# Performance work log

Hardware: AMD Instinct MI355X
Metric: run time of the kernel (lower is better)

The kernel has to match this reference:

```python
import jax, jax.numpy as jnp
import numpy as np

N_HEADS = 8
D_EMBED = 512
D_CROSS = 768
D_HEAD = D_EMBED // N_HEADS


def setup_inputs() -> dict:
    key = jax.random.key(0)
    ks = jax.random.split(key, 12)
    B, SQ, SKV = 8, 4096, 77
    s_e = 1.0 / np.sqrt(D_EMBED)
    s_c = 1.0 / np.sqrt(D_CROSS)
    return {
        "latent": jax.random.normal(ks[0], (B, SQ, D_EMBED), jnp.float32),
        "context": jax.random.normal(ks[1], (B, SKV, D_CROSS), jnp.float32),
        "wq": jax.random.normal(ks[2], (D_EMBED, D_EMBED), jnp.float32) * s_e,
        "bq": jax.random.normal(ks[3], (D_EMBED,), jnp.float32) * 0.01,
        "wk": jax.random.normal(ks[4], (D_CROSS, D_EMBED), jnp.float32) * s_c,
        "bk": jax.random.normal(ks[5], (D_EMBED,), jnp.float32) * 0.01,
        "wv": jax.random.normal(ks[6], (D_CROSS, D_EMBED), jnp.float32) * s_c,
        "bv": jax.random.normal(ks[7], (D_EMBED,), jnp.float32) * 0.01,
        "wo": jax.random.normal(ks[8], (D_EMBED, D_EMBED), jnp.float32) * s_e,
        "bo": jax.random.normal(ks[9], (D_EMBED,), jnp.float32) * 0.01,
    }


def reference(latent, context, wq, bq, wk, bk, wv, bv, wo, bo):
    B, SQ, _ = latent.shape
    SKV = context.shape[1]
    # projections; weights stored as (in, out)
    q = latent @ wq + bq                     # [B, SQ, D_EMBED]
    k = context @ wk + bk                    # [B, SKV, D_EMBED]
    v = context @ wv + bv                    # [B, SKV, D_EMBED]
    # split heads -> [B, H, S, Dh]
    q = q.reshape(B, SQ, N_HEADS, D_HEAD).transpose(0, 2, 1, 3)
    k = k.reshape(B, SKV, N_HEADS, D_HEAD).transpose(0, 2, 1, 3)
    v = v.reshape(B, SKV, N_HEADS, D_HEAD).transpose(0, 2, 1, 3)
    scale = 1.0 / np.sqrt(D_HEAD).astype(np.float32)
    w = jnp.einsum("bhqd,bhkd->bhqk", q, k) * scale  # [B, H, SQ, SKV]
    w = jax.nn.softmax(w, axis=-1)
    out = jnp.einsum("bhqk,bhkd->bhqd", w, v)        # [B, H, SQ, Dh]
    out = out.transpose(0, 2, 1, 3).reshape(B, SQ, D_EMBED)
    return out @ wo + bo
```

## Files before the change

kernel.cpp:

```cpp
#include <hip/hip_runtime.h>


typedef __attribute__((ext_vector_type(8))) __bf16 bf16x8;
typedef __attribute__((ext_vector_type(4))) float f32x4;

#define DEVI static __device__ __forceinline__

typedef __attribute__((address_space(3))) void lds_void_t;
typedef const __attribute__((address_space(1))) void gbl_void_t;
#define GLDS16(gsrc, ldst) \
  __builtin_amdgcn_global_load_lds((gbl_void_t*)(gsrc), (lds_void_t*)(ldst), 16, 0, 0)

DEVI unsigned short f2bf(float f) {
  unsigned int u = __float_as_uint(f);
  u += 0x7FFFu + ((u >> 16) & 1u);
  return (unsigned short)(u >> 16);
}

DEVI unsigned int pack2bf(float a, float b) {
  return (unsigned int)f2bf(a) | ((unsigned int)f2bf(b) << 16);
}

__global__ __launch_bounds__(256) void prep_kernel(
    const float* __restrict__ wq, const float* __restrict__ wk,
    const float* __restrict__ wv, const float* __restrict__ wo,
    unsigned short* __restrict__ wqT, unsigned short* __restrict__ wkT,
    unsigned short* __restrict__ wvT, unsigned short* __restrict__ woT,
    const float* __restrict__ latent, unsigned int* __restrict__ latBF4) {
  int bid = blockIdx.x;
  int tid = threadIdx.x;
  if (bid >= 1280) {
    size_t i = (size_t)(bid - 1280) * 256 + tid;
    const float4* in4 = (const float4*)latent;
    float4 a = in4[2 * i];
    float4 b = in4[2 * i + 1];
    uint4 o;
    o.x = pack2bf(a.x, a.y);
    o.y = pack2bf(a.z, a.w);
    o.z = pack2bf(b.x, b.y);
    o.w = pack2bf(b.z, b.w);
    *(uint4*)(latBF4 + 4 * i) = o;
    return;
  }
  __shared__ float tile[32][33];
  const float* in;
  unsigned short* out;
  int K, r;
  if (bid < 256)       { in = wq; out = wqT; K = 512; r = bid; }
  else if (bid < 640)  { in = wk; out = wkT; K = 768; r = bid - 256; }
  else if (bid < 1024) { in = wv; out = wvT; K = 768; r = bid - 640; }
  else                 { in = wo; out = woT; K = 512; r = bid - 1024; }
  int n0 = (r & 15) * 32, k0 = (r >> 4) * 32;
  int tx = tid & 31, ty = tid >> 5;
#pragma unroll
  for (int j = 0; j < 4; ++j)
    tile[ty * 4 + j][tx] = in[(size_t)(k0 + ty * 4 + j) * 512 + n0 + tx];
  __syncthreads();
#pragma unroll
  for (int j = 0; j < 4; ++j)
    out[(size_t)(n0 + ty * 4 + j) * K + k0 + tx] = f2bf(tile[tx][ty * 4 + j]);
}

__global__ __launch_bounds__(256) void kv_proj_kernel(const float* __restrict__ ctx,
                                                      const unsigned short* __restrict__ wkT,
                                                      const unsigned short* __restrict__ wvT,
                                                      const float* __restrict__ bk,
                                                      const float* __restrict__ bv,
                                                      unsigned short* __restrict__ Kp,
                                                      unsigned short* __restrict__ Vt) {
  __shared__ __align__(16) unsigned short As[64][40];
  __shared__ __align__(16) unsigned short Bs[64][40];
  int bid = blockIdx.x;
  int sel = bid / 80;
  int rem = bid % 80;
  int mt = rem / 8, nt = rem % 8;
  const unsigned short* wT = sel ? wvT : wkT;
  const float* bias = sel ? bv : bk;
  int tid = threadIdx.x;
  int l = tid & 63, w = tid >> 6;
  int lr = l & 15, lg = l >> 4;

  f32x4 acc[4] = {};
  for (int k0 = 0; k0 < 768; k0 += 32) {
#pragma unroll
    for (int it = 0; it < 2; ++it) {
      int idx4 = it * 256 + tid;
      int r = idx4 >> 3, q4 = idx4 & 7;
      int m = mt * 64 + r;
      float4 v = {0.f, 0.f, 0.f, 0.f};
      if (m < 616) v = *(const float4*)(ctx + (size_t)m * 768 + k0 + q4 * 4);
      ushort4 o;
      o.x = f2bf(v.x); o.y = f2bf(v.y); o.z = f2bf(v.z); o.w = f2bf(v.w);
      *(ushort4*)&As[r][q4 * 4] = o;
    }
    {
      int c = tid >> 2, q8 = tid & 3;
      *(uint4*)&Bs[c][q8 * 8] =
          *(const uint4*)(wT + (size_t)(nt * 64 + c) * 768 + k0 + q8 * 8);
    }
    __syncthreads();
    bf16x8 a = *(const bf16x8*)&As[w * 16 + lr][lg * 8];
#pragma unroll
    for (int n = 0; n < 4; ++n) {
      bf16x8 bb = *(const bf16x8*)&Bs[n * 16 + lr][lg * 8];
      acc[n] = __builtin_amdgcn_mfma_f32_16x16x32_bf16(a, bb, acc[n], 0, 0, 0);
    }
    __syncthreads();
  }
#pragma unroll
  for (int n = 0; n < 4; ++n) {
#pragma unroll
    for (int reg = 0; reg < 4; ++reg) {
      int m = mt * 64 + w * 16 + lg * 4 + reg;
      if (m < 616) {
        int bI = m / 77, s = m % 77;
        int col = nt * 64 + n * 16 + lr;
        int h = col >> 6, d = col & 63;
        float v = acc[n][reg] + bias[col];
        if (sel == 0)
          Kp[(((size_t)(bI * 8 + h)) * 80 + s) * 64 + d] = f2bf(v);
        else
          Vt[(((size_t)(bI * 8 + h)) * 64 + d) * 96 + s] = f2bf(v);
      }
    }
  }
}

#define KSTEP(t, boff)                                                        \
  {                                                                           \
    if ((t) < 15)                                                             \
      asm volatile("s_waitcnt vmcnt(4)" ::: "memory");                        \
    else                                                                      \
      asm volatile("s_waitcnt vmcnt(0)" ::: "memory");                        \
    __builtin_amdgcn_s_barrier();                                             \
    __builtin_amdgcn_sched_barrier(0);                                        \
    const unsigned short* bufA = smem + (boff);                               \
    const unsigned short* bufB = bufA + 4096;                                 \
    bf16x8 af[4], bv8[4];                                                     \
    _Pragma("unroll") for (int m = 0; m < 4; ++m)                             \
        af[m] = *(const bf16x8*)&bufA[(wr + m * 16 + lr) * 32 + lg * 8];      \
    _Pragma("unroll") for (int n = 0; n < 4; ++n)                             \
        bv8[n] = *(const bf16x8*)&bufB[(wc + n * 16 + lr) * 32 + lg * 8];     \
    asm volatile("s_waitcnt lgkmcnt(0)" ::: "memory");                        \
    __builtin_amdgcn_sched_barrier(0);                                        \
    __builtin_amdgcn_s_barrier();                                             \
    if ((t) <= 13) {                                                          \
      int nk = ((t) + 2) * 32;                                                \
      GLDS16(gA + nk, smem + (boff) + w * 1024);                              \
      GLDS16(gA + nk + 16 * 512, smem + (boff) + w * 1024 + 512);             \
      GLDS16(gB + nk, smem + (boff) + 4096 + w * 1024);                       \
      GLDS16(gB + nk + 16 * 512, smem + (boff) + 4096 + w * 1024 + 512);      \
    }                                                                         \
    _Pragma("unroll") for (int m = 0; m < 4; ++m)                             \
        _Pragma("unroll") for (int n = 0; n < 4; ++n)                         \
            acc[m][n] = __builtin_amdgcn_mfma_f32_16x16x32_bf16(              \
                af[m], bv8[n], acc[m][n], 0, 0, 0);                           \
  }

__global__ __launch_bounds__(256, 4) void qproj_attn_kernel(
    const unsigned short* __restrict__ A, const unsigned short* __restrict__ BT,
    const float* __restrict__ bias, const unsigned short* __restrict__ Kp,
    const unsigned short* __restrict__ Vt, unsigned short* __restrict__ Oq) {
  __shared__ __align__(16) unsigned short smem[18432];

  int bid = ((blockIdx.x & 7) << 7) | (blockIdx.x >> 3);
  size_t mbase = (size_t)(bid >> 2) * 128;
  int nbase = (bid & 3) * 128;
  int tid = threadIdx.x;
  int l = tid & 63, w = tid >> 6;
  int lr = l & 15, lg = l >> 4;
  int wr = (w >> 1) * 64, wc = (w & 1) * 64;

  const unsigned short* gA = A + (mbase + w * 32 + (l >> 2)) * 512 + (l & 3) * 8;
  const unsigned short* gB = BT + (size_t)(nbase + w * 32 + (l >> 2)) * 512 + (l & 3) * 8;

  GLDS16(gA, smem + w * 1024);
  GLDS16(gA + 16 * 512, smem + w * 1024 + 512);
  GLDS16(gB, smem + 4096 + w * 1024);
  GLDS16(gB + 16 * 512, smem + 4096 + w * 1024 + 512);
  GLDS16(gA + 32, smem + 8192 + w * 1024);
  GLDS16(gA + 32 + 16 * 512, smem + 8192 + w * 1024 + 512);
  GLDS16(gB + 32, smem + 12288 + w * 1024);
  GLDS16(gB + 32 + 16 * 512, smem + 12288 + w * 1024 + 512);

  f32x4 acc[4][4] = {};
#pragma unroll 1
  for (int t = 0; t < 16; t += 2) {
    KSTEP(t, 0);
    KSTEP(t + 1, 8192);
  }

  unsigned short* Qme = smem + w * (64 * 72);
  float bb[4];
#pragma unroll
  for (int n = 0; n < 4; ++n) bb[n] = bias[nbase + wc + n * 16 + lr];
#pragma unroll
  for (int m = 0; m < 4; ++m)
#pragma unroll
    for (int n = 0; n < 4; ++n)
#pragma unroll
      for (int reg = 0; reg < 4; ++reg)
        Qme[(m * 16 + lg * 4 + reg) * 72 + n * 16 + lr] = f2bf(acc[m][n][reg] + bb[n]);

  bf16x8 qf[4][2];
#pragma unroll
  for (int rg = 0; rg < 4; ++rg) {
    qf[rg][0] = *(const bf16x8*)&Qme[(rg * 16 + lr) * 72 + lg * 8];
    qf[rg][1] = *(const bf16x8*)&Qme[(rg * 16 + lr) * 72 + 32 + lg * 8];
  }

  unsigned short* Pme = Qme;
  for (int z = l; z < 256; z += 64) Pme[(z >> 4) * 104 + 80 + (z & 15)] = 0;

  int b = (int)(mbase >> 12);
  int h = (bid & 3) * 2 + (w & 1);
  const unsigned short* Kph = Kp + (size_t)(b * 8 + h) * (80 * 64);
  const unsigned short* Vth = Vt + (size_t)(b * 8 + h) * (64 * 96);

  const float C = 0.125f * 1.44269504088896f;

  auto QK = [&](int rg, f32x4* s) {
#pragma unroll
    for (int t = 0; t < 5; ++t) {
      const unsigned short* kr = Kph + (t * 16 + lr) * 64 + lg * 8;
      bf16x8 k0 = *(const bf16x8*)kr;
      bf16x8 k1 = *(const bf16x8*)(kr + 32);
      s[t] = __builtin_amdgcn_mfma_f32_16x16x32_bf16(qf[rg][0], k0, s[t], 0, 0, 0);
      s[t] = __builtin_amdgcn_mfma_f32_16x16x32_bf16(qf[rg][1], k1, s[t], 0, 0, 0);
    }
    if (lr >= 13) {
      s[4][0] = -1e30f; s[4][1] = -1e30f; s[4][2] = -1e30f; s[4][3] = -1e30f;
    }
  };

  f32x4 sc[5] = {};
  QK(0, sc);
#pragma unroll
  for (int rg = 0; rg < 4; ++rg) {
    float mx[4];
#pragma unroll
    for (int r = 0; r < 4; ++r)
      mx[r] = fmaxf(fmaxf(fmaxf(sc[0][r], sc[1][r]), fmaxf(sc[2][r], sc[3][r])), sc[4][r]);
#pragma unroll
    for (int d = 1; d < 16; d <<= 1)
#pragma unroll
      for (int r = 0; r < 4; ++r) mx[r] = fmaxf(mx[r], __shfl_xor(mx[r], d, 64));
    float p[5][4];
#pragma unroll
    for (int t = 0; t < 5; ++t)
#pragma unroll
      for (int r = 0; r < 4; ++r) p[t][r] = exp2f((sc[t][r] - mx[r]) * C);
#pragma unroll
    for (int t = 0; t < 5; ++t)
#pragma unroll
      for (int r = 0; r < 4; ++r)
        Pme[(lg * 4 + r) * 104 + t * 16 + lr] = f2bf(p[t][r]);

    float sm[4];
#pragma unroll
    for (int r = 0; r < 4; ++r)
      sm[r] = p[0][r] + p[1][r] + p[2][r] + p[3][r] + p[4][r];
#pragma unroll
    for (int d = 1; d < 16; d <<= 1)
#pragma unroll
      for (int r = 0; r < 4; ++r) sm[r] += __shfl_xor(sm[r], d, 64);
    float rs[4];
#pragma unroll
    for (int r = 0; r < 4; ++r) rs[r] = 1.0f / sm[r];

    f32x4 sn[5] = {};
    if (rg < 3) QK(rg + 1, sn);

    bf16x8 ap[3];
#pragma unroll
    for (int c = 0; c < 3; ++c) ap[c] = *(const bf16x8*)&Pme[lr * 104 + c * 32 + lg * 8];
#pragma unroll
    for (int ct = 0; ct < 4; ++ct) {
      f32x4 o = {};
#pragma unroll
      for (int c = 0; c < 3; ++c) {
        bf16x8 vv = *(const bf16x8*)(Vth + (size_t)(ct * 16 + lr) * 96 + c * 32 + lg * 8);
        o = __builtin_amdgcn_mfma_f32_16x16x32_bf16(ap[c], vv, o, 0, 0, 0);
      }
#pragma unroll
      for (int reg = 0; reg < 4; ++reg)
        Oq[(mbase + wr + rg * 16 + lg * 4 + reg) * 512 + nbase + wc + ct * 16 + lr] =
            f2bf(o[reg] * rs[reg]);
    }
#pragma unroll
    for (int t = 0; t < 5; ++t) sc[t] = sn[t];
  }
}

__global__ __launch_bounds__(256) void gemm512_glds_kernel(
    const unsigned short* __restrict__ A, const unsigned short* __restrict__ BT,
    const float* __restrict__ bias, float* __restrict__ Out) {
  __shared__ __align__(16) unsigned short smem[16384];
  int bid = ((blockIdx.x & 7) << 7) | (blockIdx.x >> 3);
  size_t mbase = (size_t)(bid >> 2) * 128;
  int nbase = (bid & 3) * 128;
  int tid = threadIdx.x;
  int l = tid & 63, w = tid >> 6;
  int lr = l & 15, lg = l >> 4;
  int wr = (w >> 1) * 64, wc = (w & 1) * 64;

  const unsigned short* gA = A + (mbase + w * 32 + (l >> 2)) * 512 + (l & 3) * 8;
  const unsigned short* gB = BT + (size_t)(nbase + w * 32 + (l >> 2)) * 512 + (l & 3) * 8;

  GLDS16(gA, smem + w * 1024);
  GLDS16(gA + 16 * 512, smem + w * 1024 + 512);
  GLDS16(gB, smem + 4096 + w * 1024);
  GLDS16(gB + 16 * 512, smem + 4096 + w * 1024 + 512);
  GLDS16(gA + 32, smem + 8192 + w * 1024);
  GLDS16(gA + 32 + 16 * 512, smem + 8192 + w * 1024 + 512);
  GLDS16(gB + 32, smem + 12288 + w * 1024);
  GLDS16(gB + 32 + 16 * 512, smem + 12288 + w * 1024 + 512);

  f32x4 acc[4][4] = {};
#pragma unroll 1
  for (int t = 0; t < 16; t += 2) {
    KSTEP(t, 0);
    KSTEP(t + 1, 8192);
  }

#pragma unroll
  for (int m = 0; m < 4; ++m) {
#pragma unroll
    for (int n = 0; n < 4; ++n) {
#pragma unroll
      for (int reg = 0; reg < 4; ++reg) {
        size_t row = mbase + wr + m * 16 + lg * 4 + reg;
        int col = nbase + wc + n * 16 + lr;
        Out[row * 512 + col] = acc[m][n][reg] + bias[col];
      }
    }
  }
}

static const size_t OFF_Q   = 0;
static const size_t OFF_KP  = 33554432;
static const size_t OFF_VT  = OFF_KP + 655360;
static const size_t OFF_WQT = OFF_VT + 786432;
static const size_t OFF_WKT = OFF_WQT + 524288;
static const size_t OFF_WVT = OFF_WKT + 786432;
static const size_t OFF_WOT = OFF_WVT + 786432;
static const size_t WS_NEEDED = OFF_WOT + 524288;

extern "C" void kernel_launch(void* const* d_in, const int* in_sizes, int n_in,
                              void* d_out, int out_size, void* d_ws, size_t ws_size,
                              hipStream_t stream) {
  (void)in_sizes; (void)n_in; (void)out_size;
  if (ws_size < WS_NEEDED) return;

  const float* latent  = (const float*)d_in[0];
  const float* context = (const float*)d_in[1];
  const float* wq = (const float*)d_in[2];
  const float* bq = (const float*)d_in[3];
  const float* wk = (const float*)d_in[4];
  const float* bk = (const float*)d_in[5];
  const float* wv = (const float*)d_in[6];
  const float* bv = (const float*)d_in[7];
  const float* wo = (const float*)d_in[8];
  const float* bo = (const float*)d_in[9];
  float* out = (float*)d_out;

  char* ws = (char*)d_ws;
  unsigned short* wsQ = (unsigned short*)(ws + OFF_Q);
  unsigned short* Kp  = (unsigned short*)(ws + OFF_KP);
  unsigned short* Vt  = (unsigned short*)(ws + OFF_VT);
  unsigned short* wqT = (unsigned short*)(ws + OFF_WQT);
  unsigned short* wkT = (unsigned short*)(ws + OFF_WKT);
  unsigned short* wvT = (unsigned short*)(ws + OFF_WVT);
  unsigned short* woT = (unsigned short*)(ws + OFF_WOT);

  unsigned short* latBF = (unsigned short*)d_out;

  prep_kernel<<<1280 + 8192, 256, 0, stream>>>(wq, wk, wv, wo, wqT, wkT, wvT,
                                               woT, latent,
                                               (unsigned int*)latBF);
  hipMemsetAsync(ws + OFF_KP, 0, 655360 + 786432, stream);
  kv_proj_kernel<<<160, 256, 0, stream>>>(context, wkT, wvT, bk, bv, Kp, Vt);
  qproj_attn_kernel<<<1024, 256, 0, stream>>>(latBF, wqT, bq, Kp, Vt, wsQ);
  gemm512_glds_kernel<<<1024, 256, 0, stream>>>(wsQ, woT, bo, out);
}
```

Measured before the change: 125.1 us.

## Fuse latent fp32-to-bf16 conversion into Q-projection GEMM load path

Removes the separate pass that converted the whole latent tensor to bf16 (a read of 64MB fp32 and a write of 32MB bf16). The Q-projection attention kernel now streams fp32 latent tiles straight into LDS and converts them to bf16 in registers with the hardware packed-convert instruction just before the MFMAs. The cost is double the LDS footprint for the A tile, larger shared memory per block, and occupancy lowered from 4 to 3 blocks per CU. It also adds more LDS read traffic per k-step.

```diff
diff --git a/kernel.cpp b/kernel.cpp
--- a/kernel.cpp
+++ b/kernel.cpp
@@ -17,32 +17,29 @@
   return (unsigned short)(u >> 16);
 }
 
-DEVI unsigned int pack2bf(float a, float b) {
-  return (unsigned int)f2bf(a) | ((unsigned int)f2bf(b) << 16);
-}
-
-__global__ __launch_bounds__(256) void prep_kernel(
+DEVI unsigned int cvt_pk_bf16(float lo, float hi) {
+  unsigned int r;
+  asm("v_cvt_pk_bf16_f32 %0, %1, %2" : "=v"(r) : "v"(lo), "v"(hi));
+  return r;
+}
+
+DEVI bf16x8 cvt8(float4 a, float4 b) {
+  uint4 u;
+  u.x = cvt_pk_bf16(a.x, a.y);
+  u.y = cvt_pk_bf16(a.z, a.w);
+  u.z = cvt_pk_bf16(b.x, b.y);
+  u.w = cvt_pk_bf16(b.z, b.w);
+  return *(bf16x8*)&u;
+}
+
+__global__ __launch_bounds__(256) void wtrans_all_kernel(
     const float* __restrict__ wq, const float* __restrict__ wk,
     const float* __restrict__ wv, const float* __restrict__ wo,
     unsigned short* __restrict__ wqT, unsigned short* __restrict__ wkT,
-    unsigned short* __restrict__ wvT, unsigned short* __restrict__ woT,
-    const float* __restrict__ latent, unsigned int* __restrict__ latBF4) {
+    unsigned short* __restrict__ wvT, unsigned short* __restrict__ woT) {
+  __shared__ float tile[32][33];
   int bid = blockIdx.x;
   int tid = threadIdx.x;
-  if (bid >= 1280) {
-    size_t i = (size_t)(bid - 1280) * 256 + tid;
-    const float4* in4 = (const float4*)latent;
-    float4 a = in4[2 * i];
-    float4 b = in4[2 * i + 1];
-    uint4 o;
-    o.x = pack2bf(a.x, a.y);
-    o.y = pack2bf(a.z, a.w);
-    o.z = pack2bf(b.x, b.y);
-    o.w = pack2bf(b.z, b.w);
-    *(uint4*)(latBF4 + 4 * i) = o;
-    return;
-  }
-  __shared__ float tile[32][33];
   const float* in;
   unsigned short* out;
   int K, r;
@@ -123,6 +120,178 @@
           Vt[(((size_t)(bI * 8 + h)) * 64 + d) * 96 + s] = f2bf(v);
       }
     }
+  }
+}
+
+#define QSTEP(t, AO, BO)                                                      \
+  {                                                                           \
+    if ((t) < 15)                                                             \
+      asm volatile("s_waitcnt vmcnt(6)" ::: "memory");                        \
+    else                                                                      \
+      asm volatile("s_waitcnt vmcnt(0)" ::: "memory");                        \
+    __builtin_amdgcn_s_barrier();                                             \
+    __builtin_amdgcn_sched_barrier(0);                                        \
+    const float* Af = (const float*)(smem + (AO));                            \
+    const unsigned short* Bf = smem + (BO);                                   \
+    float4 ax[4], ay[4];                                                      \
+    bf16x8 bv8[4];                                                            \
+    _Pragma("unroll") for (int m = 0; m < 4; ++m) {                           \
+      ax[m] = *(const float4*)&Af[(wr + m * 16 + lr) * 32 + lg * 8];          \
+      ay[m] = *(const float4*)&Af[(wr + m * 16 + lr) * 32 + lg * 8 + 4];      \
+    }                                                                         \
+    _Pragma("unroll") for (int n = 0; n < 4; ++n)                             \
+        bv8[n] = *(const bf16x8*)&Bf[(wc + n * 16 + lr) * 32 + lg * 8];       \
+    asm volatile("s_waitcnt lgkmcnt(0)" ::: "memory");                        \
+    __builtin_amdgcn_sched_barrier(0);                                        \
+    __builtin_amdgcn_s_barrier();                                             \
+    if ((t) <= 13) {                                                          \
+      int nk = ((t) + 2) * 32;                                                \
+      _Pragma("unroll") for (int i = 0; i < 4; ++i)                           \
+          GLDS16(gA32 + nk + i * 4096, smem + (AO) + w * 2048 + i * 512);     \
+      GLDS16(gB + nk, smem + (BO) + w * 1024);                                \
+      GLDS16(gB + nk + 16 * 512, smem + (BO) + w * 1024 + 512);               \
+    }                                                                         \
+    bf16x8 af[4];                                                             \
+    _Pragma("unroll") for (int m = 0; m < 4; ++m) af[m] = cvt8(ax[m], ay[m]); \
+    _Pragma("unroll") for (int m = 0; m < 4; ++m)                             \
+        _Pragma("unroll") for (int n = 0; n < 4; ++n)                         \
+            acc[m][n] = __builtin_amdgcn_mfma_f32_16x16x32_bf16(              \
+                af[m], bv8[n], acc[m][n], 0, 0, 0);                           \
+  }
+
+__global__ __launch_bounds__(256, 3) void qproj_attn_kernel(
+    const float* __restrict__ A32, const unsigned short* __restrict__ BT,
+    const float* __restrict__ bias, const unsigned short* __restrict__ Kp,
+    const unsigned short* __restrict__ Vt, unsigned short* __restrict__ Oq) {
+  __shared__ __align__(16) unsigned short smem[24576];
+
+  int bid = ((blockIdx.x & 7) << 7) | (blockIdx.x >> 3);
+  size_t mbase = (size_t)(bid >> 2) * 128;
+  int nbase = (bid & 3) * 128;
+  int tid = threadIdx.x;
+  int l = tid & 63, w = tid >> 6;
+  int lr = l & 15, lg = l >> 4;
+  int wr = (w >> 1) * 64, wc = (w & 1) * 64;
+
+  const float* gA32 = A32 + (mbase + w * 32 + (l >> 3)) * 512 + (l & 7) * 4;
+  const unsigned short* gB = BT + (size_t)(nbase + w * 32 + (l >> 2)) * 512 + (l & 3) * 8;
+
+#pragma unroll
+  for (int i = 0; i < 4; ++i) GLDS16(gA32 + i * 4096, smem + w * 2048 + i * 512);
+  GLDS16(gB, smem + 8192 + w * 1024);
+  GLDS16(gB + 16 * 512, smem + 8192 + w * 1024 + 512);
+#pragma unroll
+  for (int i = 0; i < 4; ++i)
+    GLDS16(gA32 + 32 + i * 4096, smem + 12288 + w * 2048 + i * 512);
+  GLDS16(gB + 32, smem + 20480 + w * 1024);
+  GLDS16(gB + 32 + 16 * 512, smem + 20480 + w * 1024 + 512);
+
+  f32x4 acc[4][4] = {};
+#pragma unroll 1
+  for (int t = 0; t < 16; t += 2) {
+    QSTEP(t, 0, 8192);
+    QSTEP(t + 1, 12288, 20480);
+  }
+
+  unsigned short* Qme = smem + w * (64 * 72);
+  float bb[4];
+#pragma unroll
+  for (int n = 0; n < 4; ++n) bb[n] = bias[nbase + wc + n * 16 + lr];
+#pragma unroll
+  for (int m = 0; m < 4; ++m)
+#pragma unroll
+    for (int n = 0; n < 4; ++n)
+#pragma unroll
+      for (int reg = 0; reg < 4; ++reg)
+        Qme[(m * 16 + lg * 4 + reg) * 72 + n * 16 + lr] = f2bf(acc[m][n][reg] + bb[n]);
+
+  bf16x8 qf[4][2];
+#pragma unroll
+  for (int rg = 0; rg < 4; ++rg) {
+    qf[rg][0] = *(const bf16x8*)&Qme[(rg * 16 + lr) * 72 + lg * 8];
+    qf[rg][1] = *(const bf16x8*)&Qme[(rg * 16 + lr) * 72 + 32 + lg * 8];
+  }
+
+  unsigned short* Pme = Qme;
+  for (int z = l; z < 256; z += 64) Pme[(z >> 4) * 104 + 80 + (z & 15)] = 0;
+
+  int b = (int)(mbase >> 12);
+  int h = (bid & 3) * 2 + (w & 1);
+  const unsigned short* Kph = Kp + (size_t)(b * 8 + h) * (80 * 64);
+  const unsigned short* Vth = Vt + (size_t)(b * 8 + h) * (64 * 96);
+
+  const float C = 0.125f * 1.44269504088896f;
+
+  auto QK = [&](int rg, f32x4* s) {
+#pragma unroll
+    for (int t = 0; t < 5; ++t) {
+      const unsigned short* kr = Kph + (t * 16 + lr) * 64 + lg * 8;
+      bf16x8 k0 = *(const bf16x8*)kr;
+      bf16x8 k1 = *(const bf16x8*)(kr + 32);
+      s[t] = __builtin_amdgcn_mfma_f32_16x16x32_bf16(qf[rg][0], k0, s[t], 0, 0, 0);
+      s[t] = __builtin_amdgcn_mfma_f32_16x16x32_bf16(qf[rg][1], k1, s[t], 0, 0, 0);
+    }
+    if (lr >= 13) {
+      s[4][0] = -1e30f; s[4][1] = -1e30f; s[4][2] = -1e30f; s[4][3] = -1e30f;
+    }
+  };
+
+  f32x4 sc[5] = {};
+  QK(0, sc);
+#pragma unroll
+  for (int rg = 0; rg < 4; ++rg) {
+    float mx[4];
+#pragma unroll
+    for (int r = 0; r < 4; ++r)
+      mx[r] = fmaxf(fmaxf(fmaxf(sc[0][r], sc[1][r]), fmaxf(sc[2][r], sc[3][r])), sc[4][r]);
+#pragma unroll
+    for (int d = 1; d < 16; d <<= 1)
+#pragma unroll
+      for (int r = 0; r < 4; ++r) mx[r] = fmaxf(mx[r], __shfl_xor(mx[r], d, 64));
+    float p[5][4];
+#pragma unroll
+    for (int t = 0; t < 5; ++t)
+#pragma unroll
+      for (int r = 0; r < 4; ++r) p[t][r] = exp2f((sc[t][r] - mx[r]) * C);
+#pragma unroll
+    for (int t = 0; t < 5; ++t)
+#pragma unroll
+      for (int r = 0; r < 4; ++r)
+        Pme[(lg * 4 + r) * 104 + t * 16 + lr] = f2bf(p[t][r]);
+
+    float sm[4];
+#pragma unroll
+    for (int r = 0; r < 4; ++r)
+      sm[r] = p[0][r] + p[1][r] + p[2][r] + p[3][r] + p[4][r];
+#pragma unroll
+    for (int d = 1; d < 16; d <<= 1)
+#pragma unroll
+      for (int r = 0; r < 4; ++r) sm[r] += __shfl_xor(sm[r], d, 64);
+    float rs[4];
+#pragma unroll
+    for (int r = 0; r < 4; ++r) rs[r] = 1.0f / sm[r];
+
+    f32x4 sn[5] = {};
+    if (rg < 3) QK(rg + 1, sn);
+
+    bf16x8 ap[3];
+#pragma unroll
+    for (int c = 0; c < 3; ++c) ap[c] = *(const bf16x8*)&Pme[lr * 104 + c * 32 + lg * 8];
+#pragma unroll
+    for (int ct = 0; ct < 4; ++ct) {
+      f32x4 o = {};
+#pragma unroll
+      for (int c = 0; c < 3; ++c) {
+        bf16x8 vv = *(const bf16x8*)(Vth + (size_t)(ct * 16 + lr) * 96 + c * 32 + lg * 8);
+        o = __builtin_amdgcn_mfma_f32_16x16x32_bf16(ap[c], vv, o, 0, 0, 0);
+      }
+#pragma unroll
+      for (int reg = 0; reg < 4; ++reg)
+        Oq[(mbase + wr + rg * 16 + lg * 4 + reg) * 512 + nbase + wc + ct * 16 + lr] =
+            f2bf(o[reg] * rs[reg]);
+    }
+#pragma unroll
+    for (int t = 0; t < 5; ++t) sc[t] = sn[t];
   }
 }
 
@@ -157,141 +326,6 @@
                 af[m], bv8[n], acc[m][n], 0, 0, 0);                           \
   }
 
-__global__ __launch_bounds__(256, 4) void qproj_attn_kernel(
-    const unsigned short* __restrict__ A, const unsigned short* __restrict__ BT,
-    const float* __restrict__ bias, const unsigned short* __restrict__ Kp,
-    const unsigned short* __restrict__ Vt, unsigned short* __restrict__ Oq) {
-  __shared__ __align__(16) unsigned short smem[18432];
-
-  int bid = ((blockIdx.x & 7) << 7) | (blockIdx.x >> 3);
-  size_t mbase = (size_t)(bid >> 2) * 128;
-  int nbase = (bid & 3) * 128;
-  int tid = threadIdx.x;
-  int l = tid & 63, w = tid >> 6;
-  int lr = l & 15, lg = l >> 4;
-  int wr = (w >> 1) * 64, wc = (w & 1) * 64;
-
-  const unsigned short* gA = A + (mbase + w * 32 + (l >> 2)) * 512 + (l & 3) * 8;
-  const unsigned short* gB = BT + (size_t)(nbase + w * 32 + (l >> 2)) * 512 + (l & 3) * 8;
-
-  GLDS16(gA, smem + w * 1024);
-  GLDS16(gA + 16 * 512, smem + w * 1024 + 512);
-  GLDS16(gB, smem + 4096 + w * 1024);
-  GLDS16(gB + 16 * 512, smem + 4096 + w * 1024 + 512);
-  GLDS16(gA + 32, smem + 8192 + w * 1024);
-  GLDS16(gA + 32 + 16 * 512, smem + 8192 + w * 1024 + 512);
-  GLDS16(gB + 32, smem + 12288 + w * 1024);
-  GLDS16(gB + 32 + 16 * 512, smem + 12288 + w * 1024 + 512);
-
-  f32x4 acc[4][4] = {};
-#pragma unroll 1
-  for (int t = 0; t < 16; t += 2) {
-    KSTEP(t, 0);
-    KSTEP(t + 1, 8192);
-  }
-
-  unsigned short* Qme = smem + w * (64 * 72);
-  float bb[4];
-#pragma unroll
-  for (int n = 0; n < 4; ++n) bb[n] = bias[nbase + wc + n * 16 + lr];
-#pragma unroll
-  for (int m = 0; m < 4; ++m)
-#pragma unroll
-    for (int n = 0; n < 4; ++n)
-#pragma unroll
-      for (int reg = 0; reg < 4; ++reg)
-        Qme[(m * 16 + lg * 4 + reg) * 72 + n * 16 + lr] = f2bf(acc[m][n][reg] + bb[n]);
-
-  bf16x8 qf[4][2];
-#pragma unroll
-  for (int rg = 0; rg < 4; ++rg) {
-    qf[rg][0] = *(const bf16x8*)&Qme[(rg * 16 + lr) * 72 + lg * 8];
-    qf[rg][1] = *(const bf16x8*)&Qme[(rg * 16 + lr) * 72 + 32 + lg * 8];
-  }
-
-  unsigned short* Pme = Qme;
-  for (int z = l; z < 256; z += 64) Pme[(z >> 4) * 104 + 80 + (z & 15)] = 0;
-
-  int b = (int)(mbase >> 12);
-  int h = (bid & 3) * 2 + (w & 1);
-  const unsigned short* Kph = Kp + (size_t)(b * 8 + h) * (80 * 64);
-  const unsigned short* Vth = Vt + (size_t)(b * 8 + h) * (64 * 96);
-
-  const float C = 0.125f * 1.44269504088896f;
-
-  auto QK = [&](int rg, f32x4* s) {
-#pragma unroll
-    for (int t = 0; t < 5; ++t) {
-      const unsigned short* kr = Kph + (t * 16 + lr) * 64 + lg * 8;
-      bf16x8 k0 = *(const bf16x8*)kr;
-      bf16x8 k1 = *(const bf16x8*)(kr + 32);
-      s[t] = __builtin_amdgcn_mfma_f32_16x16x32_bf16(qf[rg][0], k0, s[t], 0, 0, 0);
-      s[t] = __builtin_amdgcn_mfma_f32_16x16x32_bf16(qf[rg][1], k1, s[t], 0, 0, 0);
-    }
-    if (lr >= 13) {
-      s[4][0] = -1e30f; s[4][1] = -1e30f; s[4][2] = -1e30f; s[4][3] = -1e30f;
-    }
-  };
-
-  f32x4 sc[5] = {};
-  QK(0, sc);
-#pragma unroll
-  for (int rg = 0; rg < 4; ++rg) {
-    float mx[4];
-#pragma unroll
-    for (int r = 0; r < 4; ++r)
-      mx[r] = fmaxf(fmaxf(fmaxf(sc[0][r], sc[1][r]), fmaxf(sc[2][r], sc[3][r])), sc[4][r]);
-#pragma unroll
-    for (int d = 1; d < 16; d <<= 1)
-#pragma unroll
-      for (int r = 0; r < 4; ++r) mx[r] = fmaxf(mx[r], __shfl_xor(mx[r], d, 64));
-    float p[5][4];
-#pragma unroll
-    for (int t = 0; t < 5; ++t)
-#pragma unroll
-      for (int r = 0; r < 4; ++r) p[t][r] = exp2f((sc[t][r] - mx[r]) * C);
-#pragma unroll
-    for (int t = 0; t < 5; ++t)
-#pragma unroll
-      for (int r = 0; r < 4; ++r)
-        Pme[(lg * 4 + r) * 104 + t * 16 + lr] = f2bf(p[t][r]);
-
-    float sm[4];
-#pragma unroll
-    for (int r = 0; r < 4; ++r)
-      sm[r] = p[0][r] + p[1][r] + p[2][r] + p[3][r] + p[4][r];
-#pragma unroll
-    for (int d = 1; d < 16; d <<= 1)
-#pragma unroll
-      for (int r = 0; r < 4; ++r) sm[r] += __shfl_xor(sm[r], d, 64);
-    float rs[4];
-#pragma unroll
-    for (int r = 0; r < 4; ++r) rs[r] = 1.0f / sm[r];
-
-    f32x4 sn[5] = {};
-    if (rg < 3) QK(rg + 1, sn);
-
-    bf16x8 ap[3];
-#pragma unroll
-    for (int c = 0; c < 3; ++c) ap[c] = *(const bf16x8*)&Pme[lr * 104 + c * 32 + lg * 8];
-#pragma unroll
-    for (int ct = 0; ct < 4; ++ct) {
-      f32x4 o = {};
-#pragma unroll
-      for (int c = 0; c < 3; ++c) {
-        bf16x8 vv = *(const bf16x8*)(Vth + (size_t)(ct * 16 + lr) * 96 + c * 32 + lg * 8);
-        o = __builtin_amdgcn_mfma_f32_16x16x32_bf16(ap[c], vv, o, 0, 0, 0);
-      }
-#pragma unroll
-      for (int reg = 0; reg < 4; ++reg)
-        Oq[(mbase + wr + rg * 16 + lg * 4 + reg) * 512 + nbase + wc + ct * 16 + lr] =
-            f2bf(o[reg] * rs[reg]);
-    }
-#pragma unroll
-    for (int t = 0; t < 5; ++t) sc[t] = sn[t];
-  }
-}
-
 __global__ __launch_bounds__(256) void gemm512_glds_kernel(
     const unsigned short* __restrict__ A, const unsigned short* __restrict__ BT,
     const float* __restrict__ bias, float* __restrict__ Out) {
@@ -373,13 +407,10 @@
   unsigned short* wvT = (unsigned short*)(ws + OFF_WVT);
   unsigned short* woT = (unsigned short*)(ws + OFF_WOT);
 
-  unsigned short* latBF = (unsigned short*)d_out;
-
-  prep_kernel<<<1280 + 8192, 256, 0, stream>>>(wq, wk, wv, wo, wqT, wkT, wvT,
-                                               woT, latent,
-                                               (unsigned int*)latBF);
+  wtrans_all_kernel<<<1280, 256, 0, stream>>>(wq, wk, wv, wo,
+                                              wqT, wkT, wvT, woT);
   hipMemsetAsync(ws + OFF_KP, 0, 655360 + 786432, stream);
   kv_proj_kernel<<<160, 256, 0, stream>>>(context, wkT, wvT, bk, bv, Kp, Vt);
-  qproj_attn_kernel<<<1024, 256, 0, stream>>>(latBF, wqT, bq, Kp, Vt, wsQ);
+  qproj_attn_kernel<<<1024, 256, 0, stream>>>(latent, wqT, bq, Kp, Vt, wsQ);
   gemm512_glds_kernel<<<1024, 256, 0, stream>>>(wsQ, woT, bo, out);
 }
```

Measured after the change: 119.4 us. 4.6% less time.

## XOR-swizzle LDS tiles in GEMMs and overlap latent conversion with KV projection

Applied to the files above, without the earlier changes.

Global-to-LDS loads and the MFMA fragment reads now use an XOR swizzle on the 16-byte column chunk. This is meant to cut LDS bank conflicts in the two 512-wide GEMM kernels. The latent fp32-to-bf16 conversion moves out of the weight-transpose kernel and into the KV projection launch. The 160 small KV-projection blocks therefore share a grid with the 8192 conversion blocks instead of running alone on a mostly idle GPU. The swizzle has to match exactly between writer lane mapping and reader indexing, or the results will be wrong.

```diff
diff --git a/kernel.cpp b/kernel.cpp
--- a/kernel.cpp
+++ b/kernel.cpp
@@ -21,16 +21,42 @@
   return (unsigned int)f2bf(a) | ((unsigned int)f2bf(b) << 16);
 }
 
-__global__ __launch_bounds__(256) void prep_kernel(
+__global__ __launch_bounds__(256) void wtrans_all_kernel(
     const float* __restrict__ wq, const float* __restrict__ wk,
     const float* __restrict__ wv, const float* __restrict__ wo,
     unsigned short* __restrict__ wqT, unsigned short* __restrict__ wkT,
-    unsigned short* __restrict__ wvT, unsigned short* __restrict__ woT,
-    const float* __restrict__ latent, unsigned int* __restrict__ latBF4) {
+    unsigned short* __restrict__ wvT, unsigned short* __restrict__ woT) {
+  __shared__ float tile[32][33];
   int bid = blockIdx.x;
   int tid = threadIdx.x;
-  if (bid >= 1280) {
-    size_t i = (size_t)(bid - 1280) * 256 + tid;
+  const float* in;
+  unsigned short* out;
+  int K, r;
+  if (bid < 256)       { in = wq; out = wqT; K = 512; r = bid; }
+  else if (bid < 640)  { in = wk; out = wkT; K = 768; r = bid - 256; }
+  else if (bid < 1024) { in = wv; out = wvT; K = 768; r = bid - 640; }
+  else                 { in = wo; out = woT; K = 512; r = bid - 1024; }
+  int n0 = (r & 15) * 32, k0 = (r >> 4) * 32;
+  int tx = tid & 31, ty = tid >> 5;
+#pragma unroll
+  for (int j = 0; j < 4; ++j)
+    tile[ty * 4 + j][tx] = in[(size_t)(k0 + ty * 4 + j) * 512 + n0 + tx];
+  __syncthreads();
+#pragma unroll
+  for (int j = 0; j < 4; ++j)
+    out[(size_t)(n0 + ty * 4 + j) * K + k0 + tx] = f2bf(tile[tx][ty * 4 + j]);
+}
+
+__global__ __launch_bounds__(256) void kv_cvt_kernel(
+    const float* __restrict__ ctx, const unsigned short* __restrict__ wkT,
+    const unsigned short* __restrict__ wvT, const float* __restrict__ bk,
+    const float* __restrict__ bv, unsigned short* __restrict__ Kp,
+    unsigned short* __restrict__ Vt, const float* __restrict__ latent,
+    unsigned int* __restrict__ latBF4) {
+  int bid0 = blockIdx.x;
+  int tid = threadIdx.x;
+  if (bid0 >= 160) {
+    size_t i = (size_t)(bid0 - 160) * 256 + tid;
     const float4* in4 = (const float4*)latent;
     float4 a = in4[2 * i];
     float4 b = in4[2 * i + 1];
@@ -42,41 +68,14 @@
     *(uint4*)(latBF4 + 4 * i) = o;
     return;
   }
-  __shared__ float tile[32][33];
-  const float* in;
-  unsigned short* out;
-  int K, r;
-  if (bid < 256)       { in = wq; out = wqT; K = 512; r = bid; }
-  else if (bid < 640)  { in = wk; out = wkT; K = 768; r = bid - 256; }
-  else if (bid < 1024) { in = wv; out = wvT; K = 768; r = bid - 640; }
-  else                 { in = wo; out = woT; K = 512; r = bid - 1024; }
-  int n0 = (r & 15) * 32, k0 = (r >> 4) * 32;
-  int tx = tid & 31, ty = tid >> 5;
-#pragma unroll
-  for (int j = 0; j < 4; ++j)
-    tile[ty * 4 + j][tx] = in[(size_t)(k0 + ty * 4 + j) * 512 + n0 + tx];
-  __syncthreads();
-#pragma unroll
-  for (int j = 0; j < 4; ++j)
-    out[(size_t)(n0 + ty * 4 + j) * K + k0 + tx] = f2bf(tile[tx][ty * 4 + j]);
-}
-
-__global__ __launch_bounds__(256) void kv_proj_kernel(const float* __restrict__ ctx,
-                                                      const unsigned short* __restrict__ wkT,
-                                                      const unsigned short* __restrict__ wvT,
-                                                      const float* __restrict__ bk,
-                                                      const float* __restrict__ bv,
-                                                      unsigned short* __restrict__ Kp,
-                                                      unsigned short* __restrict__ Vt) {
   __shared__ __align__(16) unsigned short As[64][40];
   __shared__ __align__(16) unsigned short Bs[64][40];
-  int bid = blockIdx.x;
+  int bid = bid0;
   int sel = bid / 80;
   int rem = bid % 80;
   int mt = rem / 8, nt = rem % 8;
   const unsigned short* wT = sel ? wvT : wkT;
   const float* bias = sel ? bv : bk;
-  int tid = threadIdx.x;
   int l = tid & 63, w = tid >> 6;
   int lr = l & 15, lg = l >> 4;
 
@@ -136,11 +135,14 @@
     __builtin_amdgcn_sched_barrier(0);                                        \
     const unsigned short* bufA = smem + (boff);                               \
     const unsigned short* bufB = bufA + 4096;                                 \
+    const int swB = (lr >> 1) & 3;                                            \
     bf16x8 af[4], bv8[4];                                                     \
     _Pragma("unroll") for (int m = 0; m < 4; ++m)                             \
-        af[m] = *(const bf16x8*)&bufA[(wr + m * 16 + lr) * 32 + lg * 8];      \
+        af[m] = *(const bf16x8*)&bufA[(wr + m * 16 + lr) * 32 +               \
+                                      (lg ^ swB) * 8];                        \
     _Pragma("unroll") for (int n = 0; n < 4; ++n)                             \
-        bv8[n] = *(const bf16x8*)&bufB[(wc + n * 16 + lr) * 32 + lg * 8];     \
+        bv8[n] = *(const bf16x8*)&bufB[(wc + n * 16 + lr) * 32 +              \
+                                       (lg ^ swB) * 8];                       \
     asm volatile("s_waitcnt lgkmcnt(0)" ::: "memory");                        \
     __builtin_amdgcn_sched_barrier(0);                                        \
     __builtin_amdgcn_s_barrier();                                             \
@@ -157,6 +159,16 @@
                 af[m], bv8[n], acc[m][n], 0, 0, 0);                           \
   }
 
+#define GEMM_PROLOGUE()                                                       \
+  GLDS16(gA, smem + w * 1024);                                                \
+  GLDS16(gA + 16 * 512, smem + w * 1024 + 512);                               \
+  GLDS16(gB, smem + 4096 + w * 1024);                                         \
+  GLDS16(gB + 16 * 512, smem + 4096 + w * 1024 + 512);                        \
+  GLDS16(gA + 32, smem + 8192 + w * 1024);                                    \
+  GLDS16(gA + 32 + 16 * 512, smem + 8192 + w * 1024 + 512);                   \
+  GLDS16(gB + 32, smem + 12288 + w * 1024);                                   \
+  GLDS16(gB + 32 + 16 * 512, smem + 12288 + w * 1024 + 512);
+
 __global__ __launch_bounds__(256, 4) void qproj_attn_kernel(
     const unsigned short* __restrict__ A, const unsigned short* __restrict__ BT,
     const float* __restrict__ bias, const unsigned short* __restrict__ Kp,
@@ -171,17 +183,12 @@
   int lr = l & 15, lg = l >> 4;
   int wr = (w >> 1) * 64, wc = (w & 1) * 64;
 
-  const unsigned short* gA = A + (mbase + w * 32 + (l >> 2)) * 512 + (l & 3) * 8;
-  const unsigned short* gB = BT + (size_t)(nbase + w * 32 + (l >> 2)) * 512 + (l & 3) * 8;
-
-  GLDS16(gA, smem + w * 1024);
-  GLDS16(gA + 16 * 512, smem + w * 1024 + 512);
-  GLDS16(gB, smem + 4096 + w * 1024);
-  GLDS16(gB + 16 * 512, smem + 4096 + w * 1024 + 512);
-  GLDS16(gA + 32, smem + 8192 + w * 1024);
-  GLDS16(gA + 32 + 16 * 512, smem + 8192 + w * 1024 + 512);
-  GLDS16(gB + 32, smem + 12288 + w * 1024);
-  GLDS16(gB + 32 + 16 * 512, smem + 12288 + w * 1024 + 512);
+  const unsigned short* gA = A + (mbase + w * 32 + (l >> 2)) * 512 +
+                             (((l & 3) ^ ((l >> 3) & 3))) * 8;
+  const unsigned short* gB = BT + (size_t)(nbase + w * 32 + (l >> 2)) * 512 +
+                             (((l & 3) ^ ((l >> 3) & 3))) * 8;
+
+  GEMM_PROLOGUE();
 
   f32x4 acc[4][4] = {};
 #pragma unroll 1
@@ -304,17 +311,12 @@
   int lr = l & 15, lg = l >> 4;
   int wr = (w >> 1) * 64, wc = (w & 1) * 64;
 
-  const unsigned short* gA = A + (mbase + w * 32 + (l >> 2)) * 512 + (l & 3) * 8;
-  const unsigned short* gB = BT + (size_t)(nbase + w * 32 + (l >> 2)) * 512 + (l & 3) * 8;
-
-  GLDS16(gA, smem + w * 1024);
-  GLDS16(gA + 16 * 512, smem + w * 1024 + 512);
-  GLDS16(gB, smem + 4096 + w * 1024);
-  GLDS16(gB + 16 * 512, smem + 4096 + w * 1024 + 512);
-  GLDS16(gA + 32, smem + 8192 + w * 1024);
-  GLDS16(gA + 32 + 16 * 512, smem + 8192 + w * 1024 + 512);
-  GLDS16(gB + 32, smem + 12288 + w * 1024);
-  GLDS16(gB + 32 + 16 * 512, smem + 12288 + w * 1024 + 512);
+  const unsigned short* gA = A + (mbase + w * 32 + (l >> 2)) * 512 +
+                             (((l & 3) ^ ((l >> 3) & 3))) * 8;
+  const unsigned short* gB = BT + (size_t)(nbase + w * 32 + (l >> 2)) * 512 +
+                             (((l & 3) ^ ((l >> 3) & 3))) * 8;
+
+  GEMM_PROLOGUE();
 
   f32x4 acc[4][4] = {};
 #pragma unroll 1
@@ -375,11 +377,12 @@
 
   unsigned short* latBF = (unsigned short*)d_out;
 
-  prep_kernel<<<1280 + 8192, 256, 0, stream>>>(wq, wk, wv, wo, wqT, wkT, wvT,
-                                               woT, latent,
-                                               (unsigned int*)latBF);
+  wtrans_all_kernel<<<1280, 256, 0, stream>>>(wq, wk, wv, wo,
+                                              wqT, wkT, wvT, woT);
   hipMemsetAsync(ws + OFF_KP, 0, 655360 + 786432, stream);
-  kv_proj_kernel<<<160, 256, 0, stream>>>(context, wkT, wvT, bk, bv, Kp, Vt);
+  kv_cvt_kernel<<<160 + 8192, 256, 0, stream>>>(context, wkT, wvT, bk, bv,
+                                                Kp, Vt, latent,
+                                                (unsigned int*)latBF);
   qproj_attn_kernel<<<1024, 256, 0, stream>>>(latBF, wqT, bq, Kp, Vt, wsQ);
   gemm512_glds_kernel<<<1024, 256, 0, stream>>>(wsQ, woT, bo, out);
 }
```

Result: faster. 118.2 us (-5.5%).
